# Performance work log

Measured on AMD Instinct MI355X. Metric: run time of the kernel, lower is better.

## Reference

```python
import jax, jax.numpy as jnp
import numpy as np
from jax import lax

L, E, H, V, T = 4096, 512, 512, 50000, 32
START, END = 0, 1
NEG = -10000.0


def setup_inputs() -> dict:
    key = jax.random.key(0)
    ks = jax.random.split(key, 16)
    s = 0.1  # keep activations in a sane range
    inp = {
        'sentence': jax.random.randint(ks[0], (L,), 0, V, dtype=jnp.int32),
        'embed':  jax.random.normal(ks[1], (V, E)) * s,
        'w_ih_f': jax.random.normal(ks[2], (4 * H, E)) * s,
        'w_hh_f': jax.random.normal(ks[3], (4 * H, H)) * s,
        'b_ih_f': jax.random.normal(ks[4], (4 * H,)) * s,
        'b_hh_f': jax.random.normal(ks[5], (4 * H,)) * s,
        'w_ih_b': jax.random.normal(ks[6], (4 * H, E)) * s,
        'w_hh_b': jax.random.normal(ks[7], (4 * H, H)) * s,
        'b_ih_b': jax.random.normal(ks[8], (4 * H,)) * s,
        'b_hh_b': jax.random.normal(ks[9], (4 * H,)) * s,
        'w_out':  jax.random.normal(ks[10], (T, 2 * H)) * s,
        'b_out':  jax.random.normal(ks[11], (T,)) * s,
        'h0':     jax.random.normal(ks[13], (2, H)),
        'c0':     jax.random.normal(ks[14], (2, H)),
    }
    trans = jax.random.normal(ks[12], (T, T))
    # CRF constraints: never transition into START, never leave from END
    trans = trans.at[START, :].set(NEG).at[:, END].set(NEG)
    inp['trans'] = trans
    return inp


def _lstm_dir(xs, w_ih, w_hh, b_ih, b_hh, h0, c0, reverse):
    # xs: (L, E). PyTorch gate order: i, f, g, o. Precompute input projection.
    x_proj = xs @ w_ih.T + (b_ih + b_hh)  # (L, 4H)

    def step(carry, xp):
        h, c = carry
        gates = xp + h @ w_hh.T
        i, f, g, o = jnp.split(gates, 4)
        i, f, o = jax.nn.sigmoid(i), jax.nn.sigmoid(f), jax.nn.sigmoid(o)
        g = jnp.tanh(g)
        c = f * c + i * g
        h = o * jnp.tanh(c)
        return (h, c), h

    _, hs = lax.scan(step, (h0, c0), x_proj, reverse=reverse)
    return hs  # (L, H)


def reference(sentence, embed, w_ih_f, w_hh_f, b_ih_f, b_hh_f,
              w_ih_b, w_hh_b, b_ih_b, b_hh_b, w_out, b_out, trans, h0, c0):
    xs = embed[sentence]  # (L, E)
    hs_f = _lstm_dir(xs, w_ih_f, w_hh_f, b_ih_f, b_hh_f, h0[0], c0[0], False)
    hs_b = _lstm_dir(xs, w_ih_b, w_hh_b, b_ih_b, b_hh_b, h0[1], c0[1], True)
    feats = jnp.concatenate([hs_f, hs_b], axis=1) @ w_out.T + b_out  # (L, T)

    # Viterbi forward: trans[next, prev]
    init_v = jnp.full((T,), NEG).at[START].set(0.0)

    def vstep(fv, feat):
        scores = trans + fv[None, :]          # (T_next, T_prev)
        bptr = jnp.argmax(scores, axis=1)     # (T,)
        fv_new = jnp.max(scores, axis=1) + feat
        return fv_new, bptr

    fv, bptrs = lax.scan(vstep, init_v, feats)  # bptrs: (L, T)
    terminal = fv + trans[END]
    score = jnp.max(terminal)
    last_tag = jnp.argmax(terminal)

    # Backtrace (reverse scan): path[L-1]=last_tag, path[i]=bptrs[i+1][path[i+1]]
    def back(tag, bp):
        return bp[tag], tag

    _, path = lax.scan(back, last_tag, bptrs, reverse=True)  # (L,)
    return score, path
```

## Files before the change

kernel.cpp:

```cpp
#include <hip/hip_runtime.h>
#include <stdint.h>

#define L_SEQ 4096
#define E_DIM 512
#define H_DIM 512
#define G_DIM 2048
#define NTAG  32
#define RING_SLOTS 4

typedef unsigned long long u64;
typedef unsigned short     u16;
typedef unsigned char      u8;

__device__ __forceinline__ float bf2f(u16 u) {
    union { unsigned int i; float f; } v; v.i = ((unsigned int)u) << 16; return v.f;
}
__device__ __forceinline__ bool sniff_f32(const void* trans_raw) {
    const u16* p = (const u16*)trans_raw;
    return p[0] != p[1];
}
__device__ __forceinline__ float ldf(const void* base, long idx, bool isf32) {
    if (isf32) return ((const float*)base)[idx];
    return bf2f(((const u16*)base)[idx]);
}
__device__ __forceinline__ void unpack8_bf16(const u16* src, float* dst) {
    uint4 p = *(const uint4*)src;
    dst[0] = __uint_as_float(p.x << 16); dst[1] = __uint_as_float(p.x & 0xffff0000u);
    dst[2] = __uint_as_float(p.y << 16); dst[3] = __uint_as_float(p.y & 0xffff0000u);
    dst[4] = __uint_as_float(p.z << 16); dst[5] = __uint_as_float(p.z & 0xffff0000u);
    dst[6] = __uint_as_float(p.w << 16); dst[7] = __uint_as_float(p.w & 0xffff0000u);
}

#define LOG2E 1.44269504088896340736f
__device__ __forceinline__ float fsig(float x) {
    return __builtin_amdgcn_rcpf(1.f + __builtin_amdgcn_exp2f(-x * LOG2E));
}
__device__ __forceinline__ float ftanh(float x) {
    return 1.f - 2.f * __builtin_amdgcn_rcpf(1.f + __builtin_amdgcn_exp2f(x * (2.f * LOG2E)));
}

__global__ __launch_bounds__(256) void k_xproj(
    const int* __restrict__ sent, const void* __restrict__ embed,
    const void* __restrict__ w_ih_f, const void* __restrict__ b_ih_f, const void* __restrict__ b_hh_f,
    const void* __restrict__ w_ih_b, const void* __restrict__ b_ih_b, const void* __restrict__ b_hh_b,
    const void* __restrict__ trans_raw,
    float* __restrict__ xp_f, float* __restrict__ xp_b,
    int* __restrict__ ctrl)
{
    if (blockIdx.x == 0 && blockIdx.y == 0 && threadIdx.x == 0) {
        ctrl[4] = ctrl[4] + 8192;
    }
    const bool isf32 = sniff_f32(trans_raw);
    const int dir = (int)blockIdx.y;
    const void* W  = dir ? w_ih_b : w_ih_f;
    const void* bi = dir ? b_ih_b : b_ih_f;
    const void* bh = dir ? b_hh_b : b_hh_f;
    float* xp = dir ? xp_b : xp_f;
    const int m0 = (int)blockIdx.x * 16;
    const int tid = (int)threadIdx.x;

    __shared__ float xs[16][520];
    __shared__ float wl[16][520];

    {
        const int r = tid >> 4, c0 = (tid & 15) * 32;
        const long row = sent[m0 + r];
        if (isf32) {
            const float* src = (const float*)embed + row * E_DIM + c0;
            #pragma unroll
            for (int i = 0; i < 32; i += 4) *(float4*)&xs[r][c0 + i] = *(const float4*)(src + i);
        } else {
            const u16* src = (const u16*)embed + row * E_DIM + c0;
            #pragma unroll
            for (int i = 0; i < 32; i += 8) unpack8_bf16(src + i, &xs[r][c0 + i]);
        }
    }
    __syncthreads();

    const int mi = tid >> 4, gi = tid & 15;
    for (int gb = 0; gb < 128; ++gb) {
        const int g0 = gb * 16;
        {
            const int r = tid >> 4, c0 = (tid & 15) * 32;
            if (isf32) {
                const float* src = (const float*)W + (long)(g0 + r) * E_DIM + c0;
                #pragma unroll
                for (int i = 0; i < 32; i += 4) *(float4*)&wl[r][c0 + i] = *(const float4*)(src + i);
            } else {
                const u16* src = (const u16*)W + (long)(g0 + r) * E_DIM + c0;
                #pragma unroll
                for (int i = 0; i < 32; i += 8) unpack8_bf16(src + i, &wl[r][c0 + i]);
            }
        }
        __syncthreads();

        float acc = 0.f;
        #pragma unroll 4
        for (int k = 0; k < E_DIM; k += 4) {
            const float4 xv = *(const float4*)&xs[mi][k];
            const float4 wv = *(const float4*)&wl[gi][k];
            acc = fmaf(xv.x, wv.x, acc); acc = fmaf(xv.y, wv.y, acc);
            acc = fmaf(xv.z, wv.z, acc); acc = fmaf(xv.w, wv.w, acc);
        }
        const int g = g0 + gi;
        const float bias = ldf(bi, g, isf32) + ldf(bh, g, isf32);
        xp[(long)(m0 + mi) * G_DIM + g] = acc + bias;
        __syncthreads();
    }
}

__global__ __launch_bounds__(256, 1) void k_lstm(
    const void* __restrict__ w_hh_f, const void* __restrict__ w_hh_b,
    const void* __restrict__ h0, const void* __restrict__ c0,
    const void* __restrict__ trans_raw,
    const float* __restrict__ xp_f, const float* __restrict__ xp_b,
    float* __restrict__ hs_f, float* __restrict__ hs_b,
    u64* __restrict__ ring_f, u64* __restrict__ ring_b,
    const int* __restrict__ ctrl)
{
    const bool isf32 = sniff_f32(trans_raw);
    const int dir = (int)(blockIdx.x >> 5);
    const int wg  = (int)(blockIdx.x & 31);
    const int j0  = wg * 16;
    const unsigned salt = (unsigned)ctrl[4];
    const void* Whh = dir ? w_hh_b : w_hh_f;
    const float* xp = dir ? xp_b : xp_f;
    float* hs       = dir ? hs_b : hs_f;
    u64* ring       = dir ? ring_b : ring_f;

    const int tid = (int)threadIdx.x;
    const int rp  = tid >> 3;
    const int ks  = tid & 7;
    const int d   = rp >> 1;
    const int gp  = rp & 1;
    const int g0r = gp * 2;

    __shared__ float h_lds[512 + 32];

    float wreg[2][64];
    #pragma unroll
    for (int rl = 0; rl < 2; ++rl) {
        const long roff = (long)((g0r + rl) * H_DIM + j0 + d) * H_DIM + ks * 64;
        if (isf32) {
            const float* wrow = (const float*)Whh + roff;
            #pragma unroll
            for (int b = 0; b < 16; ++b) *(float4*)&wreg[rl][b * 4] = *(const float4*)(wrow + b * 4);
        } else {
            const u16* wrow = (const u16*)Whh + roff;
            #pragma unroll
            for (int b = 0; b < 8; ++b) unpack8_bf16(wrow + b * 8, &wreg[rl][b * 8]);
        }
    }

    {
        const int w0 = tid * 2;
        h_lds[w0 + ((w0 >> 6) << 2)]     = ldf(h0, dir * H_DIM + w0, isf32);
        h_lds[w0 + 1 + ((w0 >> 6) << 2)] = ldf(h0, dir * H_DIM + w0 + 1, isf32);
    }

    const bool is_act = ((tid & 15) == 0);
    const int  jown   = j0 + d;
    float cst = 0.f;
    if (is_act) cst = ldf(c0, dir * H_DIM + jown, isf32);

    const int b16 = tid >> 4, off = tid & 15;
    const int pidx = is_act ? -1 : (b16 * 15 + off - 1);
    int jw0 = 0, jw1 = 0, jw2 = -1;
    if (pidx >= 0) {
        const int w0 = 2 * pidx, w1 = 2 * pidx + 1;
        jw0 = w0 + (w0 >= j0 ? 16 : 0);
        jw1 = w1 + (w1 >= j0 ? 16 : 0);
        if (pidx < 16) { const int w2 = 480 + pidx; jw2 = w2 + (w2 >= j0 ? 16 : 0); }
    }

    int t = dir ? (L_SEQ - 1) : 0;
    float xc0 = 0, xc1 = 0, xc2 = 0, xc3 = 0, xn0 = 0, xn1 = 0, xn2 = 0, xn3 = 0;
    if (is_act) {
        const float* xr = xp + (long)t * G_DIM + jown;
        xn0 = xr[0]; xn1 = xr[H_DIM]; xn2 = xr[2 * H_DIM]; xn3 = xr[3 * H_DIM];
    }
    __syncthreads();

    #pragma unroll 1
    for (int k = 0; k < L_SEQ; ++k) {
        t = dir ? (L_SEQ - 1 - k) : k;
        const long rb = (long)(k & (RING_SLOTS - 1)) * H_DIM;
        const unsigned tagv = salt + (unsigned)(k + 1);

        if (is_act) {
            xc0 = xn0; xc1 = xn1; xc2 = xn2; xc3 = xn3;
            if (k + 1 < L_SEQ) {
                const int nt = dir ? (t - 1) : (t + 1);
                const float* xr = xp + (long)nt * G_DIM + jown;
                xn0 = xr[0]; xn1 = xr[H_DIM]; xn2 = xr[2 * H_DIM]; xn3 = xr[3 * H_DIM];
            }
        }

        float a0 = 0, a1 = 0;
        const float4* hb = (const float4*)(h_lds + ks * 68);
        #pragma unroll
        for (int q = 0; q < 16; ++q) {
            const float4 hv = hb[q];
            a0 = fmaf(wreg[0][4*q+0], hv.x, a0); a0 = fmaf(wreg[0][4*q+1], hv.y, a0);
            a0 = fmaf(wreg[0][4*q+2], hv.z, a0); a0 = fmaf(wreg[0][4*q+3], hv.w, a0);
            a1 = fmaf(wreg[1][4*q+0], hv.x, a1); a1 = fmaf(wreg[1][4*q+1], hv.y, a1);
            a1 = fmaf(wreg[1][4*q+2], hv.z, a1); a1 = fmaf(wreg[1][4*q+3], hv.w, a1);
        }
        #pragma unroll
        for (int m = 1; m < 8; m <<= 1) { a0 += __shfl_xor(a0, m); a1 += __shfl_xor(a1, m); }
        const float b0 = __shfl_xor(a0, 8);
        const float b1 = __shfl_xor(a1, 8);

        if (is_act) {
            const float iv = fsig(a0 + xc0);
            const float fo = fsig(a1 + xc1);
            const float gv = ftanh(b0 + xc2);
            const float ov = fsig(b1 + xc3);
            cst = fo * cst + iv * gv;
            const float hv2 = ov * ftanh(cst);
            h_lds[jown + ((jown >> 6) << 2)] = hv2;
            hs[(long)t * H_DIM + jown] = hv2;
            const u64 pk = (((u64)tagv) << 32) | (u64)__float_as_uint(hv2);
            __hip_atomic_store(&ring[rb + jown], pk,
                               __ATOMIC_RELAXED, __HIP_MEMORY_SCOPE_AGENT);
        }

        if (k + 1 < L_SEQ && pidx >= 0) {
            u64* pa0 = &ring[rb + jw0];
            u64* pa1 = &ring[rb + jw1];
            u64* pa2 = (jw2 >= 0) ? &ring[rb + jw2] : pa0;
            u64 v0 = 0, v1 = 0, v2 = 0;
            bool q0 = false, q1 = false, q2 = (jw2 < 0);
            do {
                if (!q0) { v0 = __hip_atomic_load(pa0, __ATOMIC_RELAXED, __HIP_MEMORY_SCOPE_AGENT); }
                if (!q1) { v1 = __hip_atomic_load(pa1, __ATOMIC_RELAXED, __HIP_MEMORY_SCOPE_AGENT); }
                if (!q2) { v2 = __hip_atomic_load(pa2, __ATOMIC_RELAXED, __HIP_MEMORY_SCOPE_AGENT); }
                q0 = q0 || ((unsigned)(v0 >> 32) == tagv);
                q1 = q1 || ((unsigned)(v1 >> 32) == tagv);
                q2 = q2 || ((unsigned)(v2 >> 32) == tagv);
            } while (!(q0 && q1 && q2));
            h_lds[jw0 + ((jw0 >> 6) << 2)] = __uint_as_float((unsigned)v0);
            h_lds[jw1 + ((jw1 >> 6) << 2)] = __uint_as_float((unsigned)v1);
            if (jw2 >= 0) h_lds[jw2 + ((jw2 >> 6) << 2)] = __uint_as_float((unsigned)v2);
        }
        __syncthreads();
    }
}

__global__ __launch_bounds__(256) void k_feats(
    const float* __restrict__ hs_f, const float* __restrict__ hs_b,
    const void* __restrict__ w_out, const void* __restrict__ b_out,
    const void* __restrict__ trans_raw, float* __restrict__ feats)
{
    const bool isf32 = sniff_f32(trans_raw);
    const int n  = (int)threadIdx.x & 31;
    const int tl = (int)threadIdx.x >> 5;
    const int t  = (int)blockIdx.x * 8 + tl;
    const float* hf = hs_f + (long)t * H_DIM;
    const float* hb = hs_b + (long)t * H_DIM;
    float acc = ldf(b_out, n, isf32);
    if (isf32) {
        const float* wf = (const float*)w_out + (long)n * 1024;
        const float* wb = wf + 512;
        #pragma unroll 4
        for (int j = 0; j < 512; j += 4) {
            const float4 hv = *(const float4*)&hf[j];
            const float4 wv = *(const float4*)&wf[j];
            acc = fmaf(hv.x, wv.x, acc); acc = fmaf(hv.y, wv.y, acc);
            acc = fmaf(hv.z, wv.z, acc); acc = fmaf(hv.w, wv.w, acc);
            const float4 hv2 = *(const float4*)&hb[j];
            const float4 wv2 = *(const float4*)&wb[j];
            acc = fmaf(hv2.x, wv2.x, acc); acc = fmaf(hv2.y, wv2.y, acc);
            acc = fmaf(hv2.z, wv2.z, acc); acc = fmaf(hv2.w, wv2.w, acc);
        }
    } else {
        const u16* wfh = (const u16*)w_out + (long)n * 1024;
        const u16* wbh = wfh + 512;
        #pragma unroll 2
        for (int j = 0; j < 512; j += 8) {
            float wt[8];
            unpack8_bf16(&wfh[j], wt);
            const float4 h0v = *(const float4*)&hf[j];
            const float4 h1v = *(const float4*)&hf[j + 4];
            acc = fmaf(h0v.x, wt[0], acc); acc = fmaf(h0v.y, wt[1], acc);
            acc = fmaf(h0v.z, wt[2], acc); acc = fmaf(h0v.w, wt[3], acc);
            acc = fmaf(h1v.x, wt[4], acc); acc = fmaf(h1v.y, wt[5], acc);
            acc = fmaf(h1v.z, wt[6], acc); acc = fmaf(h1v.w, wt[7], acc);
            unpack8_bf16(&wbh[j], wt);
            const float4 h2v = *(const float4*)&hb[j];
            const float4 h3v = *(const float4*)&hb[j + 4];
            acc = fmaf(h2v.x, wt[0], acc); acc = fmaf(h2v.y, wt[1], acc);
            acc = fmaf(h2v.z, wt[2], acc); acc = fmaf(h2v.w, wt[3], acc);
            acc = fmaf(h3v.x, wt[4], acc); acc = fmaf(h3v.y, wt[5], acc);
            acc = fmaf(h3v.z, wt[6], acc); acc = fmaf(h3v.w, wt[7], acc);
        }
    }
    feats[(long)t * 32 + n] = acc;
}

__global__ __launch_bounds__(64) void k_viterbi(
    const float* __restrict__ feats, const void* __restrict__ trans_raw,
    u8* __restrict__ bptr, float* __restrict__ out)
{
    const bool isf32 = sniff_f32(trans_raw);
    const int lane = (int)threadIdx.x;
    const int n = lane & 31, half = lane >> 5;
    __shared__ u8 mlds[64 * 32];
    __shared__ u8 entry[64];

    float tr[16];
    #pragma unroll
    for (int i = 0; i < 16; ++i) tr[i] = ldf(trans_raw, n * 32 + half * 16 + i, isf32);
    const float tr_end = ldf(trans_raw, 32 + n, isf32);

    float fvreg = (n == 0) ? 0.f : -10000.f;
    float fnext = feats[n];
    #pragma unroll 1
    for (int tt = 0; tt < L_SEQ; ++tt) {
        const float fcur = fnext;
        const int nt = (tt + 1 < L_SEQ) ? tt + 1 : tt;
        fnext = feats[(long)nt * 32 + n];

        float best = -3.4e38f; int bp = 0;
        #pragma unroll
        for (int i = 0; i < 16; ++i) {
            const float c = tr[i] + __shfl(fvreg, half * 16 + i);
            if (c > best) { best = c; bp = half * 16 + i; }
        }
        const float ob = __shfl_xor(best, 32);
        const int  obp = __shfl_xor(bp, 32);
        if (ob > best || (ob == best && obp < bp)) { best = ob; bp = obp; }

        fvreg = best + fcur;
        if (half == 0) bptr[(long)tt * 32 + n] = (u8)bp;
    }

    float term = (half == 0) ? (fvreg + tr_end) : -3.4e38f;
    int   ti   = (half == 0) ? n : 1000;
    #pragma unroll
    for (int m = 1; m < 64; m <<= 1) {
        const float ov = __shfl_xor(term, m);
        const int   oi = __shfl_xor(ti, m);
        if (ov > term || (ov == term && oi < ti)) { term = ov; ti = oi; }
    }
    if (lane == 0) out[0] = term;
    __syncthreads();

    unsigned cur[32];
    #pragma unroll
    for (int ch = 0; ch < 32; ++ch) cur[ch] = (unsigned)ch;
    const int cbase = lane * 64;
    for (int s = 63; s >= 0; --s) {
        const u8* row = bptr + (long)(cbase + s) * 32;
        #pragma unroll
        for (int ch = 0; ch < 32; ++ch) cur[ch] = row[cur[ch]];
    }
    #pragma unroll
    for (int ch = 0; ch < 32; ++ch) mlds[lane * 32 + ch] = (u8)cur[ch];
    __syncthreads();

    if (lane == 0) {
        int tag = ti;
        for (int c = 63; c >= 0; --c) { entry[c] = (u8)tag; tag = mlds[c * 32 + tag]; }
    }
    __syncthreads();

    {
        int tag = entry[lane];
        for (int s = 63; s >= 0; --s) {
            const int gidx = cbase + s;
            out[1 + gidx] = (float)tag;
            tag = bptr[(long)gidx * 32 + tag];
        }
    }
}

extern "C" void kernel_launch(void* const* d_in, const int* in_sizes, int n_in,
                              void* d_out, int out_size, void* d_ws, size_t ws_size,
                              hipStream_t stream)
{
    (void)in_sizes; (void)n_in; (void)out_size; (void)ws_size;
    const int* sent  = (const int*)d_in[0];
    const void* embed  = d_in[1];
    const void* w_ih_f = d_in[2];
    const void* w_hh_f = d_in[3];
    const void* b_ih_f = d_in[4];
    const void* b_hh_f = d_in[5];
    const void* w_ih_b = d_in[6];
    const void* w_hh_b = d_in[7];
    const void* b_ih_b = d_in[8];
    const void* b_hh_b = d_in[9];
    const void* w_out  = d_in[10];
    const void* b_out  = d_in[11];
    const void* h0     = d_in[12];
    const void* c0     = d_in[13];
    const void* trans  = d_in[14];

    char* ws = (char*)d_ws;
    float* xp_f  = (float*)(ws);
    float* xp_b  = (float*)(ws + (32ull << 20));
    float* hs_f  = (float*)(ws + (64ull << 20));
    float* hs_b  = (float*)(ws + (72ull << 20));
    u64*   ring_f = (u64*)(ws + (80ull << 20));
    u64*   ring_b = (u64*)(ws + (80ull << 20) + (64u << 10));
    int*   ctrl   = (int*)(ws + (80ull << 20) + (128u << 10));
    float* feats = (float*)(ws);
    u8*    bptr  = (u8*)(ws + (1ull << 20));

    k_xproj<<<dim3(256, 2), 256, 0, stream>>>(sent, embed,
        w_ih_f, b_ih_f, b_hh_f, w_ih_b, b_ih_b, b_hh_b, trans, xp_f, xp_b, ctrl);
    k_lstm<<<64, 256, 0, stream>>>(w_hh_f, w_hh_b, h0, c0, trans, xp_f, xp_b,
                                   hs_f, hs_b, ring_f, ring_b, ctrl);
    k_feats<<<512, 256, 0, stream>>>(hs_f, hs_b, w_out, b_out, trans, feats);
    k_viterbi<<<1, 64, 0, stream>>>(feats, trans, bptr, (float*)d_out);
}
```

Baseline: 12.57 ms.

## Add dedicated poller wavefronts and double-buffered LDS for LSTM h exchange

```diff
diff --git a/kernel.cpp b/kernel.cpp
--- a/kernel.cpp
+++ b/kernel.cpp
@@ -109,7 +109,7 @@
     }
 }
 
-__global__ __launch_bounds__(256, 1) void k_lstm(
+__global__ __launch_bounds__(320, 1) void k_lstm(
     const void* __restrict__ w_hh_f, const void* __restrict__ w_hh_b,
     const void* __restrict__ h0, const void* __restrict__ c0,
     const void* __restrict__ trans_raw,
@@ -129,49 +129,39 @@
     u64* ring       = dir ? ring_b : ring_f;
 
     const int tid = (int)threadIdx.x;
+    const bool is_cmp = (tid < 256);
     const int rp  = tid >> 3;
     const int ks  = tid & 7;
     const int d   = rp >> 1;
     const int gp  = rp & 1;
     const int g0r = gp * 2;
 
-    __shared__ float h_lds[512 + 32];
+    __shared__ float h_lds[2][512 + 32];
 
     float wreg[2][64];
-    #pragma unroll
-    for (int rl = 0; rl < 2; ++rl) {
-        const long roff = (long)((g0r + rl) * H_DIM + j0 + d) * H_DIM + ks * 64;
-        if (isf32) {
-            const float* wrow = (const float*)Whh + roff;
-            #pragma unroll
-            for (int b = 0; b < 16; ++b) *(float4*)&wreg[rl][b * 4] = *(const float4*)(wrow + b * 4);
-        } else {
-            const u16* wrow = (const u16*)Whh + roff;
-            #pragma unroll
-            for (int b = 0; b < 8; ++b) unpack8_bf16(wrow + b * 8, &wreg[rl][b * 8]);
-        }
-    }
-
-    {
+    if (is_cmp) {
+        #pragma unroll
+        for (int rl = 0; rl < 2; ++rl) {
+            const long roff = (long)((g0r + rl) * H_DIM + j0 + d) * H_DIM + ks * 64;
+            if (isf32) {
+                const float* wrow = (const float*)Whh + roff;
+                #pragma unroll
+                for (int b = 0; b < 16; ++b) *(float4*)&wreg[rl][b * 4] = *(const float4*)(wrow + b * 4);
+            } else {
+                const u16* wrow = (const u16*)Whh + roff;
+                #pragma unroll
+                for (int b = 0; b < 8; ++b) unpack8_bf16(wrow + b * 8, &wreg[rl][b * 8]);
+            }
+        }
         const int w0 = tid * 2;
-        h_lds[w0 + ((w0 >> 6) << 2)]     = ldf(h0, dir * H_DIM + w0, isf32);
-        h_lds[w0 + 1 + ((w0 >> 6) << 2)] = ldf(h0, dir * H_DIM + w0 + 1, isf32);
-    }
-
-    const bool is_act = ((tid & 15) == 0);
+        h_lds[0][w0 + ((w0 >> 6) << 2)]     = ldf(h0, dir * H_DIM + w0, isf32);
+        h_lds[0][w0 + 1 + ((w0 >> 6) << 2)] = ldf(h0, dir * H_DIM + w0 + 1, isf32);
+    }
+
+    const bool is_act = is_cmp && ((tid & 15) == 0);
     const int  jown   = j0 + d;
     float cst = 0.f;
     if (is_act) cst = ldf(c0, dir * H_DIM + jown, isf32);
-
-    const int b16 = tid >> 4, off = tid & 15;
-    const int pidx = is_act ? -1 : (b16 * 15 + off - 1);
-    int jw0 = 0, jw1 = 0, jw2 = -1;
-    if (pidx >= 0) {
-        const int w0 = 2 * pidx, w1 = 2 * pidx + 1;
-        jw0 = w0 + (w0 >= j0 ? 16 : 0);
-        jw1 = w1 + (w1 >= j0 ? 16 : 0);
-        if (pidx < 16) { const int w2 = 480 + pidx; jw2 = w2 + (w2 >= j0 ? 16 : 0); }
-    }
 
     int t = dir ? (L_SEQ - 1) : 0;
     float xc0 = 0, xc1 = 0, xc2 = 0, xc3 = 0, xn0 = 0, xn1 = 0, xn2 = 0, xn3 = 0;
@@ -179,6 +169,7 @@
         const float* xr = xp + (long)t * G_DIM + jown;
         xn0 = xr[0]; xn1 = xr[H_DIM]; xn2 = xr[2 * H_DIM]; xn3 = xr[3 * H_DIM];
     }
+    int esc = 0;
     __syncthreads();
 
     #pragma unroll 1
@@ -186,62 +177,90 @@
         t = dir ? (L_SEQ - 1 - k) : k;
         const long rb = (long)(k & (RING_SLOTS - 1)) * H_DIM;
         const unsigned tagv = salt + (unsigned)(k + 1);
-
-        if (is_act) {
-            xc0 = xn0; xc1 = xn1; xc2 = xn2; xc3 = xn3;
-            if (k + 1 < L_SEQ) {
-                const int nt = dir ? (t - 1) : (t + 1);
-                const float* xr = xp + (long)nt * G_DIM + jown;
-                xn0 = xr[0]; xn1 = xr[H_DIM]; xn2 = xr[2 * H_DIM]; xn3 = xr[3 * H_DIM];
-            }
-        }
-
-        float a0 = 0, a1 = 0;
-        const float4* hb = (const float4*)(h_lds + ks * 68);
-        #pragma unroll
-        for (int q = 0; q < 16; ++q) {
-            const float4 hv = hb[q];
-            a0 = fmaf(wreg[0][4*q+0], hv.x, a0); a0 = fmaf(wreg[0][4*q+1], hv.y, a0);
-            a0 = fmaf(wreg[0][4*q+2], hv.z, a0); a0 = fmaf(wreg[0][4*q+3], hv.w, a0);
-            a1 = fmaf(wreg[1][4*q+0], hv.x, a1); a1 = fmaf(wreg[1][4*q+1], hv.y, a1);
-            a1 = fmaf(wreg[1][4*q+2], hv.z, a1); a1 = fmaf(wreg[1][4*q+3], hv.w, a1);
-        }
-        #pragma unroll
-        for (int m = 1; m < 8; m <<= 1) { a0 += __shfl_xor(a0, m); a1 += __shfl_xor(a1, m); }
-        const float b0 = __shfl_xor(a0, 8);
-        const float b1 = __shfl_xor(a1, 8);
-
-        if (is_act) {
-            const float iv = fsig(a0 + xc0);
-            const float fo = fsig(a1 + xc1);
-            const float gv = ftanh(b0 + xc2);
-            const float ov = fsig(b1 + xc3);
-            cst = fo * cst + iv * gv;
-            const float hv2 = ov * ftanh(cst);
-            h_lds[jown + ((jown >> 6) << 2)] = hv2;
-            hs[(long)t * H_DIM + jown] = hv2;
-            const u64 pk = (((u64)tagv) << 32) | (u64)__float_as_uint(hv2);
-            __hip_atomic_store(&ring[rb + jown], pk,
-                               __ATOMIC_RELAXED, __HIP_MEMORY_SCOPE_AGENT);
-        }
-
-        if (k + 1 < L_SEQ && pidx >= 0) {
-            u64* pa0 = &ring[rb + jw0];
-            u64* pa1 = &ring[rb + jw1];
-            u64* pa2 = (jw2 >= 0) ? &ring[rb + jw2] : pa0;
-            u64 v0 = 0, v1 = 0, v2 = 0;
-            bool q0 = false, q1 = false, q2 = (jw2 < 0);
-            do {
-                if (!q0) { v0 = __hip_atomic_load(pa0, __ATOMIC_RELAXED, __HIP_MEMORY_SCOPE_AGENT); }
-                if (!q1) { v1 = __hip_atomic_load(pa1, __ATOMIC_RELAXED, __HIP_MEMORY_SCOPE_AGENT); }
-                if (!q2) { v2 = __hip_atomic_load(pa2, __ATOMIC_RELAXED, __HIP_MEMORY_SCOPE_AGENT); }
-                q0 = q0 || ((unsigned)(v0 >> 32) == tagv);
-                q1 = q1 || ((unsigned)(v1 >> 32) == tagv);
-                q2 = q2 || ((unsigned)(v2 >> 32) == tagv);
-            } while (!(q0 && q1 && q2));
-            h_lds[jw0 + ((jw0 >> 6) << 2)] = __uint_as_float((unsigned)v0);
-            h_lds[jw1 + ((jw1 >> 6) << 2)] = __uint_as_float((unsigned)v1);
-            if (jw2 >= 0) h_lds[jw2 + ((jw2 >> 6) << 2)] = __uint_as_float((unsigned)v2);
+        const float* hcur = h_lds[k & 1];
+        float* hnext      = h_lds[(k + 1) & 1];
+
+        if (is_cmp) {
+            if (is_act) {
+                xc0 = xn0; xc1 = xn1; xc2 = xn2; xc3 = xn3;
+                if (k + 1 < L_SEQ) {
+                    const int nt = dir ? (t - 1) : (t + 1);
+                    const float* xr = xp + (long)nt * G_DIM + jown;
+                    xn0 = xr[0]; xn1 = xr[H_DIM]; xn2 = xr[2 * H_DIM]; xn3 = xr[3 * H_DIM];
+                }
+            }
+            float a0 = 0, a1 = 0;
+            const float4* hb = (const float4*)(hcur + ks * 68);
+            #pragma unroll
+            for (int q = 0; q < 16; ++q) {
+                const float4 hv = hb[q];
+                a0 = fmaf(wreg[0][4*q+0], hv.x, a0); a0 = fmaf(wreg[0][4*q+1], hv.y, a0);
+                a0 = fmaf(wreg[0][4*q+2], hv.z, a0); a0 = fmaf(wreg[0][4*q+3], hv.w, a0);
+                a1 = fmaf(wreg[1][4*q+0], hv.x, a1); a1 = fmaf(wreg[1][4*q+1], hv.y, a1);
+                a1 = fmaf(wreg[1][4*q+2], hv.z, a1); a1 = fmaf(wreg[1][4*q+3], hv.w, a1);
+            }
+            #pragma unroll
+            for (int m = 1; m < 8; m <<= 1) { a0 += __shfl_xor(a0, m); a1 += __shfl_xor(a1, m); }
+            const float b0 = __shfl_xor(a0, 8);
+            const float b1 = __shfl_xor(a1, 8);
+
+            if (is_act) {
+                const float iv = fsig(a0 + xc0);
+                const float fo = fsig(a1 + xc1);
+                const float gv = ftanh(b0 + xc2);
+                const float ov = fsig(b1 + xc3);
+                cst = fo * cst + iv * gv;
+                const float hv2 = ov * ftanh(cst);
+                hs[(long)t * H_DIM + jown] = hv2;
+                const u64 pk = (((u64)tagv) << 32) | (u64)__float_as_uint(hv2);
+                __hip_atomic_store(&ring[rb + jown], pk,
+                                   __ATOMIC_RELAXED, __HIP_MEMORY_SCOPE_AGENT);
+            }
+        } else if (k + 1 < L_SEQ) {
+            const int l = tid - 256;
+            u64* pw = &ring[rb + 8 * l];
+            u64 v0=0,v1=0,v2=0,v3=0,v4=0,v5=0,v6=0,v7=0;
+            int spins = 0;
+            for (;;) {
+                if (!esc) {
+                    asm volatile(
+                        "global_load_dwordx2 %0, %8, off sc1\n\t"
+                        "global_load_dwordx2 %1, %8, off offset:8 sc1\n\t"
+                        "global_load_dwordx2 %2, %8, off offset:16 sc1\n\t"
+                        "global_load_dwordx2 %3, %8, off offset:24 sc1\n\t"
+                        "global_load_dwordx2 %4, %8, off offset:32 sc1\n\t"
+                        "global_load_dwordx2 %5, %8, off offset:40 sc1\n\t"
+                        "global_load_dwordx2 %6, %8, off offset:48 sc1\n\t"
+                        "global_load_dwordx2 %7, %8, off offset:56 sc1\n\t"
+                        "s_waitcnt vmcnt(0)"
+                        : "=&v"(v0), "=&v"(v1), "=&v"(v2), "=&v"(v3),
+                          "=&v"(v4), "=&v"(v5), "=&v"(v6), "=&v"(v7)
+                        : "v"(pw) : "memory");
+                    __builtin_amdgcn_sched_barrier(0);
+                    if (++spins > 4096) esc = 1;
+                } else {
+                    v0 = __hip_atomic_load(pw + 0, __ATOMIC_RELAXED, __HIP_MEMORY_SCOPE_AGENT);
+                    v1 = __hip_atomic_load(pw + 1, __ATOMIC_RELAXED, __HIP_MEMORY_SCOPE_AGENT);
+                    v2 = __hip_atomic_load(pw + 2, __ATOMIC_RELAXED, __HIP_MEMORY_SCOPE_AGENT);
+                    v3 = __hip_atomic_load(pw + 3, __ATOMIC_RELAXED, __HIP_MEMORY_SCOPE_AGENT);
+                    v4 = __hip_atomic_load(pw + 4, __ATOMIC_RELAXED, __HIP_MEMORY_SCOPE_AGENT);
+                    v5 = __hip_atomic_load(pw + 5, __ATOMIC_RELAXED, __HIP_MEMORY_SCOPE_AGENT);
+                    v6 = __hip_atomic_load(pw + 6, __ATOMIC_RELAXED, __HIP_MEMORY_SCOPE_AGENT);
+                    v7 = __hip_atomic_load(pw + 7, __ATOMIC_RELAXED, __HIP_MEMORY_SCOPE_AGENT);
+                }
+                if (((unsigned)(v0 >> 32) == tagv) && ((unsigned)(v1 >> 32) == tagv) &&
+                    ((unsigned)(v2 >> 32) == tagv) && ((unsigned)(v3 >> 32) == tagv) &&
+                    ((unsigned)(v4 >> 32) == tagv) && ((unsigned)(v5 >> 32) == tagv) &&
+                    ((unsigned)(v6 >> 32) == tagv) && ((unsigned)(v7 >> 32) == tagv)) break;
+            }
+            const int pbase = 8 * l + ((l >> 3) << 2);
+            float4 fa, fb;
+            fa.x = __uint_as_float((unsigned)v0); fa.y = __uint_as_float((unsigned)v1);
+            fa.z = __uint_as_float((unsigned)v2); fa.w = __uint_as_float((unsigned)v3);
+            fb.x = __uint_as_float((unsigned)v4); fb.y = __uint_as_float((unsigned)v5);
+            fb.z = __uint_as_float((unsigned)v6); fb.w = __uint_as_float((unsigned)v7);
+            *(float4*)&hnext[pbase]     = fa;
+            *(float4*)&hnext[pbase + 4] = fb;
         }
         __syncthreads();
     }
@@ -409,7 +428,7 @@
 
     k_xproj<<<dim3(256, 2), 256, 0, stream>>>(sent, embed,
         w_ih_f, b_ih_f, b_hh_f, w_ih_b, b_ih_b, b_hh_b, trans, xp_f, xp_b, ctrl);
-    k_lstm<<<64, 256, 0, stream>>>(w_hh_f, w_hh_b, h0, c0, trans, xp_f, xp_b,
+    k_lstm<<<64, 320, 0, stream>>>(w_hh_f, w_hh_b, h0, c0, trans, xp_f, xp_b,
                                    hs_f, hs_b, ring_f, ring_b, ctrl);
     k_feats<<<512, 256, 0, stream>>>(hs_f, hs_b, w_out, b_out, trans, feats);
     k_viterbi<<<1, 64, 0, stream>>>(feats, trans, bptr, (float*)d_out);
```

New measurement: 15.47 ms. 1.23x slower.
